# Kernel tuning notes

Measured on AMD Instinct MI355X. Metric: run time of the kernel, lower is better.

Reference implementation:

```python
import jax, jax.numpy as jnp
import numpy as np

C = 256        # in_channels == depth
HEADS = 8
K = 251        # kernel_size == attended axis length
DH = C // HEADS  # 32
EPS = 1e-5


def _bn(x, g, b, axes, ch_axis):
    # training-mode batchnorm: batch statistics, biased variance
    m = jnp.mean(x, axes, keepdims=True)
    v = jnp.var(x, axes, keepdims=True)
    shape = [1] * x.ndim
    shape[ch_axis] = -1
    return (x - m) / jnp.sqrt(v + EPS) * g.reshape(shape) + b.reshape(shape)


def _axial_cross(x, y, wk, wq, wv, gk, bk, gq, bq, gkq, bkq, glog, blog, rel):
    B, _, H, W = x.shape  # [B, C, H, W], height_dim=False -> attend over W
    # permute(0,2,1,3) then fold freq axis into batch: [B*H, C, W]
    xb = x.transpose(0, 2, 1, 3).reshape(B * H, C, W)
    yb = y.transpose(0, 2, 1, 3).reshape(B * H, C, W)
    # 1x1 conv1d == channel-mixing einsum, then BN over (batch, length)
    k = _bn(jnp.einsum('oc,bcl->bol', wk, xb), gk, bk, (0, 2), 1)
    q = _bn(jnp.einsum('oc,bcl->bol', wq, yb), gq, bq, (0, 2), 1)
    v = _bn(jnp.einsum('oc,bcl->bol', wv, xb), gkq, bkq, (0, 2), 1)  # original uses kq_bn on v
    kqv = jnp.concatenate([k, q, v], axis=1).reshape(B * H, HEADS, DH * 2, W)
    k = kqv[:, :, : DH // 2]          # [b, h, dh/2, W]
    q = kqv[:, :, DH // 2: DH]        # [b, h, dh/2, W]
    v = kqv[:, :, DH:]                # [b, h, dh,   W]
    # relative position encodings gathered by distance
    ki = jnp.arange(K)
    dist = (ki[None, :] - ki[:, None] + K - 1).reshape(-1)
    rel_e = rel[:, dist].reshape(DH * 2, K, K)
    q_enc = rel_e[: DH // 2]
    k_enc = rel_e[DH // 2: DH]
    v_enc = rel_e[DH:]
    qk = jnp.einsum('bhdx,bhdy->bhxy', q, k)
    qr = jnp.einsum('bhdx,dxy->bhxy', q, q_enc)
    kr = jnp.einsum('bhdx,dxy->bhxy', k, k_enc).transpose(0, 1, 3, 2)
    logits = jnp.concatenate([qk, qr, kr], axis=1)  # [b, 3*h, W, W]
    logits = _bn(logits, glog, blog, (0, 2, 3), 1)  # BatchNorm2d on 3*h channels
    logits = logits.reshape(B * H, 3, HEADS, W, W).sum(axis=1)
    weights = jax.nn.softmax(logits, axis=3)
    attn = jnp.einsum('bhxy,bhdy->bhdx', weights, v)        # [b, h, dh, W]
    attn_enc = jnp.einsum('bhxy,dxy->bhdx', weights, v_enc)  # [b, h, dh, W]
    attn_out = jnp.concatenate([attn, attn_enc], axis=-1)    # cat along length axis (as in original)
    attn_out = attn_out.reshape(B * H, C * 2, W)
    out = attn_out.reshape(B, H, C, 2, W).sum(axis=3)        # [B, H, C, W]
    return out.transpose(0, 2, 1, 3)                          # [B, C, H, W]


def setup_inputs() -> dict:
    key = jax.random.key(0)
    ks = jax.random.split(key, 6)
    B, H, W = 2, 15, 251
    sc = 0.05
    return {
        'x': jax.random.normal(ks[0], (B, C, H, W), jnp.float32),
        'y': jax.random.normal(ks[1], (B, C, H, W), jnp.float32),
        'wk': jax.random.normal(ks[2], (C // 2, C), jnp.float32) * sc,
        'wq': jax.random.normal(ks[3], (C // 2, C), jnp.float32) * sc,
        'wv': jax.random.normal(ks[4], (C, C), jnp.float32) * sc,
        'gk': jnp.ones((C // 2,), jnp.float32), 'bk': jnp.zeros((C // 2,), jnp.float32),
        'gq': jnp.ones((C // 2,), jnp.float32), 'bq': jnp.zeros((C // 2,), jnp.float32),
        'gkq': jnp.ones((C,), jnp.float32), 'bkq': jnp.zeros((C,), jnp.float32),
        'glog': jnp.ones((HEADS * 3,), jnp.float32), 'blog': jnp.zeros((HEADS * 3,), jnp.float32),
        'rel': jax.random.normal(ks[5], (DH * 2, 2 * K - 1), jnp.float32),
    }


def reference(x, y, wk, wq, wv, gk, bk, gq, bq, gkq, bkq, glog, blog, rel):
    return _axial_cross(x, y, wk, wq, wv, gk, bk, gq, bq, gkq, bkq, glog, blog, rel)
```

## Files before the change

### kernel.cpp

```cpp
#include <hip/hip_runtime.h>
#include <hip/hip_bf16.h>
#include <cstdint>

#define WPOS 251
#define NBB  30
#define NCH  512
#define RELP 501
#define NEPS 1e-5f

typedef _Float16 half2_t __attribute__((ext_vector_type(2)));
typedef _Float16 half8_t __attribute__((ext_vector_type(8)));
typedef float f32x16_t __attribute__((ext_vector_type(16)));

#if defined(__has_builtin)
#if __has_builtin(__builtin_amdgcn_fdot2)
#define FDOT2(a, b, c) __builtin_amdgcn_fdot2((a), (b), (c), false)
#endif
#endif
#ifndef FDOT2
#define FDOT2(a, b, c) ((float)(a)[0] * (float)(b)[0] + (float)(a)[1] * (float)(b)[1] + (c))
#endif

static constexpr size_t SZ_Z     = (size_t)NBB * NCH * WPOS;
static constexpr size_t OFF_Z    = 0;
static constexpr size_t OFF_VH   = OFF_Z + SZ_Z;
static constexpr size_t SZ_VH    = (size_t)NBB * 8 * 128 * 32;
static constexpr size_t OFF_RETC = OFF_VH + SZ_VH;
static constexpr size_t OFF_VETP = OFF_RETC + (size_t)RELP * 16;
static constexpr size_t OFF_P1Q  = OFF_VETP + (size_t)256 * 32;
static constexpr size_t OFF_P1K  = OFF_P1Q + (size_t)16 * 502;
static constexpr size_t OFF_P2Q  = OFF_P1K + (size_t)16 * 502;
static constexpr size_t OFF_P2K  = OFF_P2Q + (size_t)256 * 502;
static constexpr size_t OFF_CA   = OFF_P2K + (size_t)256 * 502;
static constexpr size_t OFF_CB   = OFF_CA + 512;
static constexpr size_t OFF_LP   = OFF_CB + 512;
static constexpr size_t OFF_LAB  = OFF_LP + (size_t)240 * 6;
static constexpr size_t OFF_LPP  = OFF_LAB + 48;

static __device__ __forceinline__ unsigned packh2(float a, float b) {
  half2_t t;
  t[0] = (_Float16)a;
  t[1] = (_Float16)b;
  return __builtin_bit_cast(unsigned, t);
}
static __device__ __forceinline__ half2_t ash2(unsigned u) {
  return __builtin_bit_cast(half2_t, u);
}

__global__ __launch_bounds__(256) void k_gemm(
    const float* __restrict__ x, const float* __restrict__ y,
    const float* __restrict__ wk, const float* __restrict__ wq,
    const float* __restrict__ wv, float* __restrict__ z) {
  int l0 = blockIdx.x * 64;
  int o0 = blockIdx.y * 64;
  int bb = blockIdx.z;
  int b = bb / 15, hi = bb % 15;
  const float* src;
  const float* wmat;
  int orow0;
  if (o0 < 128)      { wmat = wk; orow0 = o0;       src = x; }
  else if (o0 < 256) { wmat = wq; orow0 = o0 - 128; src = y; }
  else               { wmat = wv; orow0 = o0 - 256; src = x; }

  __shared__ _Float16 Ah[64][68];
  __shared__ _Float16 Bh[64][68];

  int tid = threadIdx.x;
  int lane = tid & 63, wv4 = tid >> 6;
  int wo = wv4 >> 1, wl = wv4 & 1;
  int m = lane & 31, kh = lane >> 5;

  f32x16_t acc = {};

  int cA = tid & 63, ogA = tid >> 6;
  int lB = tid & 63, kgB = tid >> 6;
  int lglob = l0 + lB;
  bool lok = (lglob < WPOS);
  const float* xcol = src + (size_t)(((size_t)b * 256) * 15 + hi) * WPOS + lglob;

  for (int c0 = 0; c0 < 256; c0 += 64) {
#pragma unroll
    for (int i = 0; i < 16; ++i) {
      int o = ogA * 16 + i;
      Ah[o][cA] = (_Float16)wmat[(size_t)(orow0 + o) * 256 + c0 + cA];
    }
#pragma unroll
    for (int i = 0; i < 16; ++i) {
      int k = kgB * 16 + i;
      float v = lok ? xcol[(size_t)(c0 + k) * 15 * WPOS] : 0.f;
      Bh[k][lB] = (_Float16)v;
    }
    __syncthreads();
#pragma unroll
    for (int ks = 0; ks < 4; ++ks) {
      const _Float16* ap = &Ah[wo * 32 + m][ks * 16 + kh * 8];
      uint2 aLo = *(const uint2*)(ap);
      uint2 aHi = *(const uint2*)(ap + 4);
      uint4 au = {aLo.x, aLo.y, aHi.x, aHi.y};
      half8_t af = __builtin_bit_cast(half8_t, au);
      half8_t bf;
      int kb = ks * 16 + kh * 8;
      int bcol = wl * 32 + m;
#pragma unroll
      for (int e = 0; e < 8; ++e) bf[e] = Bh[kb + e][bcol];
      acc = __builtin_amdgcn_mfma_f32_32x32x16_f16(af, bf, acc, 0, 0, 0);
    }
    __syncthreads();
  }

  int n = lane & 31;
  int lout = l0 + wl * 32 + n;
  if (lout < WPOS) {
#pragma unroll
    for (int r = 0; r < 16; ++r) {
      int mrow = (r & 3) + 8 * (r >> 2) + 4 * kh;
      int o = o0 + wo * 32 + mrow;
      z[((size_t)bb * NCH + o) * WPOS + lout] = acc[r];
    }
  }
}

__global__ __launch_bounds__(256) void k_chan_stats(
    const float* __restrict__ z,
    const float* __restrict__ gk, const float* __restrict__ bk,
    const float* __restrict__ gq, const float* __restrict__ bq,
    const float* __restrict__ gkq, const float* __restrict__ bkq,
    float* __restrict__ ca, float* __restrict__ cb) {
  int o = blockIdx.x;
  int tid = threadIdx.x;
  float s = 0.f, s2 = 0.f;
  for (int idx = tid; idx < NBB * WPOS; idx += 256) {
    int bb = idx / WPOS, l = idx - bb * WPOS;
    float v = z[((size_t)bb * NCH + o) * WPOS + l];
    s += v; s2 += v * v;
  }
  __shared__ float r1[256], r2[256];
  r1[tid] = s; r2[tid] = s2; __syncthreads();
  for (int st = 128; st > 0; st >>= 1) {
    if (tid < st) { r1[tid] += r1[tid + st]; r2[tid] += r2[tid + st]; }
    __syncthreads();
  }
  if (tid == 0) {
    float n = (float)(NBB * WPOS);
    float mean = r1[0] / n;
    float var = r2[0] / n - mean * mean;
    float g, bi;
    if (o < 128)      { g = gk[o];        bi = bk[o]; }
    else if (o < 256) { g = gq[o - 128];  bi = bq[o - 128]; }
    else              { g = gkq[o - 256]; bi = bkq[o - 256]; }
    float a = g / sqrtf(var + NEPS);
    ca[o] = a;
    cb[o] = bi - mean * a;
  }
}

__global__ __launch_bounds__(256) void k_norm_vh(
    const float* __restrict__ z, const float* __restrict__ ca, const float* __restrict__ cb,
    unsigned* __restrict__ vh) {
  int blk = blockIdx.x;
  int bbh = blk % 240, lt = blk / 240;
  int bb = bbh >> 3, h = bbh & 7;
  int l0 = lt * 64;
  __shared__ float T[32][65];
  int tid = threadIdx.x;
  const float* zv = z + ((size_t)bb * NCH + h * 64 + 32) * WPOS;
  for (int i = tid; i < 32 * 64; i += 256) {
    int ch = i >> 6, l = i & 63;
    int gl = l0 + l;
    int cch = h * 64 + 32 + ch;
    T[ch][l] = (gl < WPOS) ? (ca[cch] * zv[(size_t)ch * WPOS + gl] + cb[cch]) : 0.f;
  }
  __syncthreads();
  int p0 = l0 >> 1;
  for (int i = tid; i < 32 * 32; i += 256) {
    int pl = i >> 5, ch = i & 31;
    int gp = p0 + pl;
    if (gp < 128)
      vh[((size_t)bbh * 128 + gp) * 32 + ch] = packh2(T[ch][2 * pl], T[ch][2 * pl + 1]);
  }
}

__global__ void k_rel_prep(const float* __restrict__ rel, unsigned* __restrict__ retc,
                           unsigned* __restrict__ vetp) {
  int idx = blockIdx.x * 256 + threadIdx.x;
  if (idx < RELP * 16) {
    int p = idx >> 4, j = idx & 15;
    float lo, hi;
    if (j < 8) {
      lo = rel[(size_t)(2 * j) * RELP + p];
      hi = rel[(size_t)(2 * j + 1) * RELP + p];
    } else {
      int jj = j - 8;
      lo = rel[(size_t)(16 + 2 * jj) * RELP + (500 - p)];
      hi = rel[(size_t)(17 + 2 * jj) * RELP + (500 - p)];
    }
    retc[(size_t)p * 16 + j] = packh2(lo, hi);
  } else {
    int i2 = idx - RELP * 16;
    if (i2 >= 256 * 32) return;
    int t = i2 >> 5, ch = i2 & 31;
    float lo = (2 * t <= 500) ? rel[(size_t)(32 + ch) * RELP + 2 * t] : 0.f;
    float hi = (2 * t + 1 <= 500) ? rel[(size_t)(32 + ch) * RELP + 2 * t + 1] : 0.f;
    vetp[(size_t)t * 32 + ch] = packh2(lo, hi);
  }
}

__global__ __launch_bounds__(256) void k_prefix(const float* __restrict__ rel,
                                                float* __restrict__ p1q, float* __restrict__ p1k,
                                                float* __restrict__ p2q, float* __restrict__ p2k) {
  int task = blockIdx.x;
  const float* ra;
  const float* rb = nullptr;
  float* outp;
  if (task < 16)        { ra = rel + (size_t)task * RELP; outp = p1q + (size_t)task * 502; }
  else if (task < 32)   { ra = rel + (size_t)task * RELP; outp = p1k + (size_t)(task - 16) * 502; }
  else if (task < 288)  { int pr = task - 32;
                          ra = rel + (size_t)(pr >> 4) * RELP;
                          rb = rel + (size_t)(pr & 15) * RELP;
                          outp = p2q + (size_t)pr * 502; }
  else                  { int pr = task - 288;
                          ra = rel + (size_t)(16 + (pr >> 4)) * RELP;
                          rb = rel + (size_t)(16 + (pr & 15)) * RELP;
                          outp = p2k + (size_t)pr * 502; }
  __shared__ float buf[256];
  int t = threadIdx.x;
  int i0 = 2 * t, i1 = 2 * t + 1;
  float a0 = (i0 < RELP) ? (rb ? ra[i0] * rb[i0] : ra[i0]) : 0.f;
  float a1 = (i1 < RELP) ? (rb ? ra[i1] * rb[i1] : ra[i1]) : 0.f;
  buf[t] = a0 + a1;
  __syncthreads();
#pragma unroll
  for (int off = 1; off < 256; off <<= 1) {
    float v = buf[t];
    float add = (t >= off) ? buf[t - off] : 0.f;
    __syncthreads();
    buf[t] = v + add;
    __syncthreads();
  }
  float ex = buf[t] - (a0 + a1);
  if (i0 <= RELP) outp[i0] = ex;
  if (i1 <= RELP) outp[i1] = ex + a0;
}

__device__ __forceinline__ float block_reduce(float v, float* red, int tid) {
  red[tid] = v; __syncthreads();
  for (int s = 128; s > 0; s >>= 1) {
    if (tid < s) red[tid] += red[tid + s];
    __syncthreads();
  }
  float r = red[0]; __syncthreads();
  return r;
}

__global__ __launch_bounds__(256) void k_lstats1(
    const float* __restrict__ z, const float* __restrict__ ca, const float* __restrict__ cb,
    const float* __restrict__ p1q, const float* __restrict__ p1k,
    const float* __restrict__ p2q, const float* __restrict__ p2k,
    float* __restrict__ lpp) {
  int blk = blockIdx.x;
  int bbh = blk % 240, xc = blk / 240;
  int bb = bbh >> 3, h = bbh & 7;
  int x0 = xc * 64;
  int tid = threadIdx.x;
  __shared__ float qs[16][68], ks[16][68];
  __shared__ float red[256];
  const float* zb = z + ((size_t)bb * NCH + h * 64) * WPOS;
  for (int idx = tid; idx < 16 * 64; idx += 256) {
    int d = idx >> 6, xl = idx & 63;
    int xg = x0 + xl;
    float kv = 0.f, qv = 0.f;
    if (xg < WPOS) {
      int chk = h * 64 + d, chq = h * 64 + 16 + d;
      kv = ca[chk] * zb[(size_t)d * WPOS + xg] + cb[chk];
      qv = ca[chq] * zb[(size_t)(16 + d) * WPOS + xg] + cb[chq];
    }
    ks[d][xl] = kv; qs[d][xl] = qv;
  }
  __syncthreads();
  float* outp = lpp + ((size_t)bbh * 4 + xc) * 548;
  if (tid < 16) {
    float s = 0.f;
    for (int xl = 0; xl < 64; ++xl) s += qs[tid][xl];
    outp[516 + tid] = s;
  } else if (tid < 32) {
    float s = 0.f;
    for (int xl = 0; xl < 64; ++xl) s += ks[tid - 16][xl];
    outp[532 + (tid - 16)] = s;
  }
  {
    int d = tid >> 4, d2 = tid & 15;
    float g1 = 0.f, g2 = 0.f;
    for (int xl = 0; xl < 64; ++xl) {
      g1 += qs[d][xl] * qs[d2][xl];
      g2 += ks[d][xl] * ks[d2][xl];
    }
    outp[tid] = g1;
    outp[256 + tid] = g2;
  }
  float v_sumqr = 0.f, v_sqqr = 0.f, v_sumkr = 0.f, v_sqkr = 0.f;
  for (int idx = tid; idx < 16 * 64; idx += 256) {
    int d = idx >> 6, xl = idx & 63;
    int xg = x0 + xl;
    if (xg < WPOS) {
      int ihi = 501 - xg, ilo = 250 - xg;
      float qv = qs[d][xl];
      v_sumqr += qv * (p1q[d * 502 + ihi] - p1q[d * 502 + ilo]);
      float t = 0.f;
      for (int d2 = 0; d2 < 16; ++d2) {
        const float* pp = p2q + (size_t)(d * 16 + d2) * 502;
        t += qs[d2][xl] * (pp[ihi] - pp[ilo]);
      }
      v_sqqr += qv * t;
      float kv = ks[d][xl];
      v_sumkr += kv * (p1k[d * 502 + ihi] - p1k[d * 502 + ilo]);
      float t2 = 0.f;
      for (int d2 = 0; d2 < 16; ++d2) {
        const float* pp = p2k + (size_t)(d * 16 + d2) * 502;
        t2 += ks[d2][xl] * (pp[ihi] - pp[ilo]);
      }
      v_sqkr += kv * t2;
    }
  }
  float r1 = block_reduce(v_sumqr, red, tid);
  float r2 = block_reduce(v_sqqr, red, tid);
  float r3 = block_reduce(v_sumkr, red, tid);
  float r4 = block_reduce(v_sqkr, red, tid);
  if (tid == 0) { outp[512] = r1; outp[513] = r2; outp[514] = r3; outp[515] = r4; }
}

__global__ __launch_bounds__(256) void k_lstats2(const float* __restrict__ lpp,
                                                 float* __restrict__ lp) {
  int bbh = blockIdx.x;
  int tid = threadIdx.x;
  __shared__ float red[256];
  __shared__ float qsums[16], ksums[16];
  const float* b0 = lpp + (size_t)bbh * 4 * 548;
  float qg = b0[tid] + b0[548 + tid] + b0[1096 + tid] + b0[1644 + tid];
  float kg = b0[256 + tid] + b0[804 + tid] + b0[1352 + tid] + b0[1900 + tid];
  if (tid < 16) {
    qsums[tid] = b0[516 + tid] + b0[1064 + tid] + b0[1612 + tid] + b0[2160 + tid];
    ksums[tid] = b0[532 + tid] + b0[1080 + tid] + b0[1628 + tid] + b0[2176 + tid];
  }
  float sqqk = block_reduce(qg * kg, red, tid);
  if (tid == 0) {
    float sum_qk = 0.f;
    for (int d = 0; d < 16; ++d) sum_qk += qsums[d] * ksums[d];
    float s1 = 0.f, s2 = 0.f, s3 = 0.f, s4 = 0.f;
    for (int c = 0; c < 4; ++c) {
      const float* bc = b0 + (size_t)c * 548;
      s1 += bc[512]; s2 += bc[513]; s3 += bc[514]; s4 += bc[515];
    }
    float* o = lp + (size_t)bbh * 6;
    o[0] = sum_qk; o[1] = sqqk;
    o[2] = s1; o[3] = s2; o[4] = s3; o[5] = s4;
  }
}

__global__ void k_logit_final(const float* __restrict__ lp,
                              const float* __restrict__ glog, const float* __restrict__ blog,
                              float* __restrict__ lab) {
  int c = threadIdx.x;
  if (c >= 24) return;
  int grp = c >> 3, h = c & 7;
  float s = 0.f, s2 = 0.f;
  for (int bb = 0; bb < NBB; ++bb) {
    const float* o = lp + (size_t)(bb * 8 + h) * 6 + grp * 2;
    s += o[0]; s2 += o[1];
  }
  float n = (float)NBB * (float)WPOS * (float)WPOS;
  float mean = s / n;
  float var = s2 / n - mean * mean;
  float la = glog[c] / sqrtf(var + NEPS);
  lab[c * 2] = la;
  lab[c * 2 + 1] = blog[c] - mean * la;
}

__global__ __launch_bounds__(256) void k_attn(
    const float* __restrict__ z, const float* __restrict__ ca, const float* __restrict__ cb,
    const unsigned* __restrict__ vh,
    const unsigned* __restrict__ retc, const unsigned* __restrict__ vetp,
    const float* __restrict__ lab, float* __restrict__ out) {
  int blk = blockIdx.x;
  int bbh = blk % 240, tile = blk / 240;
  int bb = bbh >> 3, h = bbh & 7;
  int b = bb / 15, hi = bb % 15;
  int x0 = tile * 32;
  int nr = min(32, WPOS - x0);
  int tid = threadIdx.x;
  int lane = tid & 63, wvid = tid >> 6;

  const float LOG2E = 1.4426950408889634f;
  float la_qk = lab[h * 2] * LOG2E;
  float la_qr = lab[(8 + h) * 2] * LOG2E;
  float la_kr = lab[(16 + h) * 2] * LOG2E;

  __shared__ __align__(16) unsigned Su[32 * 132];
  __shared__ __align__(16) unsigned winU[282 * 18];
  __shared__ __align__(16) unsigned uSh[256];
  _Float16* S = (_Float16*)Su;
  unsigned* qsP = uSh;
  float* sred = (float*)uSh;
  float* Cred = (float*)winU;

  int pwin0 = 251 - x0 - nr;
  int nwin = 250 + nr;

  const float* zb = z + ((size_t)bb * NCH + h * 64) * WPOS;

  for (int i = tid; i < nwin * 16; i += 256) {
    int r = i >> 4, j = i & 15;
    winU[r * 18 + j] = retc[(size_t)(pwin0 + r) * 16 + j];
  }

  {
    int xx = tid & 31, j = tid >> 5;
    int xcl = min(x0 + xx, WPOS - 1);
    int ch0 = h * 64 + 16 + 2 * j;
    float q0 = ca[ch0]     * zb[(size_t)(16 + 2 * j) * WPOS + xcl] + cb[ch0];
    float q1 = ca[ch0 + 1] * zb[(size_t)(17 + 2 * j) * WPOS + xcl] + cb[ch0 + 1];
    qsP[xx * 8 + j] = packh2(q0, q1);
  }

  int yy = wvid * 64 + lane;
  int yc = min(yy, WPOS - 1);
  bool yok = (yy < WPOS);
  half2_t khv[8];
#pragma unroll
  for (int d = 0; d < 8; ++d) {
    int ch = h * 64 + 2 * d;
    float k0 = ca[ch]     * zb[(size_t)(2 * d) * WPOS + yc] + cb[ch];
    float k1 = ca[ch + 1] * zb[(size_t)(2 * d + 1) * WPOS + yc] + cb[ch + 1];
    khv[d] = __builtin_bit_cast(half2_t, packh2(k0, k1));
  }
  __syncthreads();

  {
    int rowbase = yc + nr - 1;
    for (int xx = 0; xx < nr; ++xx) {
      const unsigned* wr = &winU[(size_t)(rowbase - xx) * 18];
      const unsigned* qp = &qsP[xx * 8];
      float dqk = 0.f, dqr = 0.f, dkr = 0.f;
#pragma unroll
      for (int j2 = 0; j2 < 4; ++j2) {
        uint2 ue = *(const uint2*)(wr + 2 * j2);
        uint2 uk = *(const uint2*)(wr + 8 + 2 * j2);
        uint2 uq = *(const uint2*)(qp + 2 * j2);
        half2_t qe0 = ash2(ue.x), qe1 = ash2(ue.y);
        half2_t ke0 = ash2(uk.x), ke1 = ash2(uk.y);
        half2_t q0  = ash2(uq.x), q1  = ash2(uq.y);
        half2_t k0 = khv[2 * j2], k1 = khv[2 * j2 + 1];
        dqk = FDOT2(q0, k0, dqk);  dqk = FDOT2(q1, k1, dqk);
        dqr = FDOT2(q0, qe0, dqr); dqr = FDOT2(q1, qe1, dqr);
        dkr = FDOT2(k0, ke0, dkr); dkr = FDOT2(k1, ke1, dkr);
      }
      float sval = la_qk * dqk + la_qr * dqr + la_kr * dkr;
      S[xx * 264 + yy] = yok ? (_Float16)sval : (_Float16)0.f;
    }
  }
  for (int i = tid; i < 32 * 8; i += 256)
    S[(i >> 3) * 264 + 256 + (i & 7)] = (_Float16)0.f;
  if (nr < 32) {
    int ntail = (32 - nr) * 264;
    for (int i = tid; i < ntail; i += 256) S[nr * 264 + i] = (_Float16)0.f;
  }
  __syncthreads();

  int xx = lane & 31;
  int sl = wvid * 2 + (lane >> 5);
  int ylo = sl * 32;
  const unsigned* Srp = Su + xx * 132;
  {
    float m = -1e30f;
    if (sl < 7) {
#pragma unroll
      for (int pp = 0; pp < 16; ++pp) {
        half2_t hp = ash2(Srp[(ylo >> 1) + pp]);
        m = fmaxf(m, fmaxf((float)hp[0], (float)hp[1]));
      }
    } else {
#pragma unroll
      for (int pp = 0; pp < 13; ++pp) {
        half2_t hp = ash2(Srp[112 + pp]);
        m = fmaxf(m, fmaxf((float)hp[0], (float)hp[1]));
      }
      m = fmaxf(m, (float)S[xx * 264 + 250]);
    }
    sred[sl * 32 + xx] = m;
  }
  __syncthreads();
  float rowm = sred[0 * 32 + xx];
#pragma unroll
  for (int s = 1; s < 8; ++s) rowm = fmaxf(rowm, sred[s * 32 + xx]);
  __syncthreads();
  {
    float sacc = 0.f;
    unsigned* Swp = Su + xx * 132;
    if (sl < 7) {
#pragma unroll
      for (int pp = 0; pp < 16; ++pp) {
        half2_t hp = ash2(Swp[(ylo >> 1) + pp]);
        float e0 = exp2f((float)hp[0] - rowm);
        float e1 = exp2f((float)hp[1] - rowm);
        Swp[(ylo >> 1) + pp] = packh2(e0, e1);
        sacc += e0 + e1;
      }
    } else {
#pragma unroll
      for (int pp = 0; pp < 13; ++pp) {
        half2_t hp = ash2(Swp[112 + pp]);
        float e0 = exp2f((float)hp[0] - rowm);
        float e1 = exp2f((float)hp[1] - rowm);
        Swp[112 + pp] = packh2(e0, e1);
        sacc += e0 + e1;
      }
      float e = exp2f((float)S[xx * 264 + 250] - rowm);
      S[xx * 264 + 250] = (_Float16)e;
      sacc += e;
    }
    sred[sl * 32 + xx] = sacc;
  }
  __syncthreads();
  float denom = 0.f;
#pragma unroll
  for (int s = 0; s < 8; ++s) denom += sred[s * 32 + xx];

  f32x16_t acc = {};
  int xcol = lane & 31;
  int khh = lane >> 5;
  const _Float16* Srow = S + xcol * 264;
  {
    const unsigned* vhb = vh + (size_t)bbh * 128 * 32 + xcol;
#pragma unroll
    for (int ks = 0; ks < 4; ++ks) {
      int y0 = 64 * wvid + 16 * ks + 8 * khh;
      int t0 = y0 >> 1;
      uint4 au = {vhb[(size_t)(t0 + 0) * 32], vhb[(size_t)(t0 + 1) * 32],
                  vhb[(size_t)(t0 + 2) * 32], vhb[(size_t)(t0 + 3) * 32]};
      half8_t af = __builtin_bit_cast(half8_t, au);
      half8_t bf = *(const half8_t*)(Srow + y0);
      acc = __builtin_amdgcn_mfma_f32_32x32x16_f16(af, bf, acc, 0, 0, 0);
    }
    const unsigned* vpb = vetp + xcol;
    int ybase = xcol + x0 - 250;
#pragma unroll
    for (int ks = 0; ks < 8; ++ks) {
      int p0 = 128 * wvid + 16 * ks + 8 * khh;
      int t0 = p0 >> 1;
      uint4 au = {vpb[(size_t)(t0 + 0) * 32], vpb[(size_t)(t0 + 1) * 32],
                  vpb[(size_t)(t0 + 2) * 32], vpb[(size_t)(t0 + 3) * 32]};
      half8_t af = __builtin_bit_cast(half8_t, au);
      half8_t bf;
#pragma unroll
      for (int e = 0; e < 8; ++e) {
        int yv = ybase + p0 + e;
        bf[e] = ((unsigned)yv < 264u) ? Srow[yv] : (_Float16)0.f;
      }
      acc = __builtin_amdgcn_mfma_f32_32x32x16_f16(af, bf, acc, 0, 0, 0);
    }
  }

  if (wvid > 0) {
    float* cp = Cred + ((size_t)(wvid - 1) * 64 + lane) * 17;
#pragma unroll
    for (int r = 0; r < 16; ++r) cp[r] = acc[r];
  }
  __syncthreads();
  if (wvid == 0) {
#pragma unroll
    for (int w2 = 0; w2 < 3; ++w2) {
      const float* cp = Cred + ((size_t)w2 * 64 + lane) * 17;
#pragma unroll
      for (int r = 0; r < 16; ++r) acc[r] += cp[r];
    }
    if (xcol < nr) {
      float rinv = 1.0f / denom;
      int xg = x0 + xcol;
#pragma unroll
      for (int r = 0; r < 16; ++r) {
        int d = (r & 3) + 8 * (r >> 2) + 4 * khh;
        out[(((size_t)b * 256 + h * 32 + d) * 15 + hi) * WPOS + xg] = acc[r] * rinv;
      }
    }
  }
}

extern "C" void kernel_launch(void* const* d_in, const int* in_sizes, int n_in,
                              void* d_out, int out_size, void* d_ws, size_t ws_size,
                              hipStream_t stream) {
  const float* x    = (const float*)d_in[0];
  const float* y    = (const float*)d_in[1];
  const float* wk   = (const float*)d_in[2];
  const float* wq   = (const float*)d_in[3];
  const float* wv   = (const float*)d_in[4];
  const float* gk   = (const float*)d_in[5];
  const float* bk   = (const float*)d_in[6];
  const float* gq   = (const float*)d_in[7];
  const float* bq   = (const float*)d_in[8];
  const float* gkq  = (const float*)d_in[9];
  const float* bkq  = (const float*)d_in[10];
  const float* glog = (const float*)d_in[11];
  const float* blog = (const float*)d_in[12];
  const float* rel  = (const float*)d_in[13];
  float* out = (float*)d_out;
  float* ws  = (float*)d_ws;

  float* z      = ws + OFF_Z;
  unsigned* vh  = (unsigned*)(ws + OFF_VH);
  unsigned* retc= (unsigned*)(ws + OFF_RETC);
  unsigned* vetp= (unsigned*)(ws + OFF_VETP);
  float* p1q    = ws + OFF_P1Q;
  float* p1k    = ws + OFF_P1K;
  float* p2q    = ws + OFF_P2Q;
  float* p2k    = ws + OFF_P2K;
  float* ca     = ws + OFF_CA;
  float* cb     = ws + OFF_CB;
  float* lp     = ws + OFF_LP;
  float* lab    = ws + OFF_LAB;
  float* lpp    = ws + OFF_LPP;

  dim3 g1(4, 8, NBB);
  k_gemm<<<g1, 256, 0, stream>>>(x, y, wk, wq, wv, z);
  k_chan_stats<<<512, 256, 0, stream>>>(z, gk, bk, gq, bq, gkq, bkq, ca, cb);
  k_norm_vh<<<960, 256, 0, stream>>>(z, ca, cb, vh);
  k_rel_prep<<<(RELP * 16 + 256 * 32 + 255) / 256, 256, 0, stream>>>(rel, retc, vetp);
  k_prefix<<<544, 256, 0, stream>>>(rel, p1q, p1k, p2q, p2k);
  k_lstats1<<<960, 256, 0, stream>>>(z, ca, cb, p1q, p1k, p2q, p2k, lpp);
  k_lstats2<<<240, 256, 0, stream>>>(lpp, lp);
  k_logit_final<<<1, 32, 0, stream>>>(lp, glog, blog, lab);
  k_attn<<<240 * 8, 256, 0, stream>>>(z, ca, cb, vh, retc, vetp, lab, out);
}
```

Before: 113.9 us.

## Fuse BN statistics into GEMM epilogue and merge small kernels to cut launches

Per-channel sum and sum-of-squares are now computed in the GEMM epilogue via wave shuffles and atomics, which removes the separate channel-stats pass over z. The rel-prep and prefix kernels are merged into one launch, the V-normalise and logit-stats kernels are merged into k_mid, and the logit BN finalisation now happens inside k_attn using atomically accumulated totals. The kernel count drops from nine to five plus a memset. In exchange the atomics make the float sums order-nondeterministic, and each block recomputes the affine coefficients.

```diff
diff --git a/kernel.cpp b/kernel.cpp
--- a/kernel.cpp
+++ b/kernel.cpp
@@ -31,11 +31,8 @@
 static constexpr size_t OFF_P1K  = OFF_P1Q + (size_t)16 * 502;
 static constexpr size_t OFF_P2Q  = OFF_P1K + (size_t)16 * 502;
 static constexpr size_t OFF_P2K  = OFF_P2Q + (size_t)256 * 502;
-static constexpr size_t OFF_CA   = OFF_P2K + (size_t)256 * 502;
-static constexpr size_t OFF_CB   = OFF_CA + 512;
-static constexpr size_t OFF_LP   = OFF_CB + 512;
-static constexpr size_t OFF_LAB  = OFF_LP + (size_t)240 * 6;
-static constexpr size_t OFF_LPP  = OFF_LAB + 48;
+static constexpr size_t OFF_LPP  = OFF_P2K + (size_t)256 * 502;
+static constexpr size_t OFF_ACC  = OFF_LPP + (size_t)960 * 548;
 
 static __device__ __forceinline__ unsigned packh2(float a, float b) {
   half2_t t;
@@ -47,168 +44,35 @@
   return __builtin_bit_cast(half2_t, u);
 }
 
-__global__ __launch_bounds__(256) void k_gemm(
-    const float* __restrict__ x, const float* __restrict__ y,
-    const float* __restrict__ wk, const float* __restrict__ wq,
-    const float* __restrict__ wv, float* __restrict__ z) {
-  int l0 = blockIdx.x * 64;
-  int o0 = blockIdx.y * 64;
-  int bb = blockIdx.z;
-  int b = bb / 15, hi = bb % 15;
-  const float* src;
-  const float* wmat;
-  int orow0;
-  if (o0 < 128)      { wmat = wk; orow0 = o0;       src = x; }
-  else if (o0 < 256) { wmat = wq; orow0 = o0 - 128; src = y; }
-  else               { wmat = wv; orow0 = o0 - 256; src = x; }
-
-  __shared__ _Float16 Ah[64][68];
-  __shared__ _Float16 Bh[64][68];
-
-  int tid = threadIdx.x;
-  int lane = tid & 63, wv4 = tid >> 6;
-  int wo = wv4 >> 1, wl = wv4 & 1;
-  int m = lane & 31, kh = lane >> 5;
-
-  f32x16_t acc = {};
-
-  int cA = tid & 63, ogA = tid >> 6;
-  int lB = tid & 63, kgB = tid >> 6;
-  int lglob = l0 + lB;
-  bool lok = (lglob < WPOS);
-  const float* xcol = src + (size_t)(((size_t)b * 256) * 15 + hi) * WPOS + lglob;
-
-  for (int c0 = 0; c0 < 256; c0 += 64) {
-#pragma unroll
-    for (int i = 0; i < 16; ++i) {
-      int o = ogA * 16 + i;
-      Ah[o][cA] = (_Float16)wmat[(size_t)(orow0 + o) * 256 + c0 + cA];
-    }
-#pragma unroll
-    for (int i = 0; i < 16; ++i) {
-      int k = kgB * 16 + i;
-      float v = lok ? xcol[(size_t)(c0 + k) * 15 * WPOS] : 0.f;
-      Bh[k][lB] = (_Float16)v;
-    }
-    __syncthreads();
-#pragma unroll
-    for (int ks = 0; ks < 4; ++ks) {
-      const _Float16* ap = &Ah[wo * 32 + m][ks * 16 + kh * 8];
-      uint2 aLo = *(const uint2*)(ap);
-      uint2 aHi = *(const uint2*)(ap + 4);
-      uint4 au = {aLo.x, aLo.y, aHi.x, aHi.y};
-      half8_t af = __builtin_bit_cast(half8_t, au);
-      half8_t bf;
-      int kb = ks * 16 + kh * 8;
-      int bcol = wl * 32 + m;
-#pragma unroll
-      for (int e = 0; e < 8; ++e) bf[e] = Bh[kb + e][bcol];
-      acc = __builtin_amdgcn_mfma_f32_32x32x16_f16(af, bf, acc, 0, 0, 0);
-    }
-    __syncthreads();
-  }
-
-  int n = lane & 31;
-  int lout = l0 + wl * 32 + n;
-  if (lout < WPOS) {
-#pragma unroll
-    for (int r = 0; r < 16; ++r) {
-      int mrow = (r & 3) + 8 * (r >> 2) + 4 * kh;
-      int o = o0 + wo * 32 + mrow;
-      z[((size_t)bb * NCH + o) * WPOS + lout] = acc[r];
-    }
-  }
-}
-
-__global__ __launch_bounds__(256) void k_chan_stats(
-    const float* __restrict__ z,
-    const float* __restrict__ gk, const float* __restrict__ bk,
-    const float* __restrict__ gq, const float* __restrict__ bq,
-    const float* __restrict__ gkq, const float* __restrict__ bkq,
-    float* __restrict__ ca, float* __restrict__ cb) {
-  int o = blockIdx.x;
-  int tid = threadIdx.x;
-  float s = 0.f, s2 = 0.f;
-  for (int idx = tid; idx < NBB * WPOS; idx += 256) {
-    int bb = idx / WPOS, l = idx - bb * WPOS;
-    float v = z[((size_t)bb * NCH + o) * WPOS + l];
-    s += v; s2 += v * v;
-  }
-  __shared__ float r1[256], r2[256];
-  r1[tid] = s; r2[tid] = s2; __syncthreads();
-  for (int st = 128; st > 0; st >>= 1) {
-    if (tid < st) { r1[tid] += r1[tid + st]; r2[tid] += r2[tid + st]; }
-    __syncthreads();
-  }
-  if (tid == 0) {
-    float n = (float)(NBB * WPOS);
-    float mean = r1[0] / n;
-    float var = r2[0] / n - mean * mean;
-    float g, bi;
-    if (o < 128)      { g = gk[o];        bi = bk[o]; }
-    else if (o < 256) { g = gq[o - 128];  bi = bq[o - 128]; }
-    else              { g = gkq[o - 256]; bi = bkq[o - 256]; }
-    float a = g / sqrtf(var + NEPS);
-    ca[o] = a;
-    cb[o] = bi - mean * a;
-  }
-}
-
-__global__ __launch_bounds__(256) void k_norm_vh(
-    const float* __restrict__ z, const float* __restrict__ ca, const float* __restrict__ cb,
-    unsigned* __restrict__ vh) {
+__global__ __launch_bounds__(256) void k_pre(
+    const float* __restrict__ rel, unsigned* __restrict__ retc, unsigned* __restrict__ vetp,
+    float* __restrict__ p1q, float* __restrict__ p1k,
+    float* __restrict__ p2q, float* __restrict__ p2k) {
   int blk = blockIdx.x;
-  int bbh = blk % 240, lt = blk / 240;
-  int bb = bbh >> 3, h = bbh & 7;
-  int l0 = lt * 64;
-  __shared__ float T[32][65];
-  int tid = threadIdx.x;
-  const float* zv = z + ((size_t)bb * NCH + h * 64 + 32) * WPOS;
-  for (int i = tid; i < 32 * 64; i += 256) {
-    int ch = i >> 6, l = i & 63;
-    int gl = l0 + l;
-    int cch = h * 64 + 32 + ch;
-    T[ch][l] = (gl < WPOS) ? (ca[cch] * zv[(size_t)ch * WPOS + gl] + cb[cch]) : 0.f;
-  }
-  __syncthreads();
-  int p0 = l0 >> 1;
-  for (int i = tid; i < 32 * 32; i += 256) {
-    int pl = i >> 5, ch = i & 31;
-    int gp = p0 + pl;
-    if (gp < 128)
-      vh[((size_t)bbh * 128 + gp) * 32 + ch] = packh2(T[ch][2 * pl], T[ch][2 * pl + 1]);
-  }
-}
-
-__global__ void k_rel_prep(const float* __restrict__ rel, unsigned* __restrict__ retc,
-                           unsigned* __restrict__ vetp) {
-  int idx = blockIdx.x * 256 + threadIdx.x;
-  if (idx < RELP * 16) {
-    int p = idx >> 4, j = idx & 15;
-    float lo, hi;
-    if (j < 8) {
-      lo = rel[(size_t)(2 * j) * RELP + p];
-      hi = rel[(size_t)(2 * j + 1) * RELP + p];
-    } else {
-      int jj = j - 8;
-      lo = rel[(size_t)(16 + 2 * jj) * RELP + (500 - p)];
-      hi = rel[(size_t)(17 + 2 * jj) * RELP + (500 - p)];
-    }
-    retc[(size_t)p * 16 + j] = packh2(lo, hi);
-  } else {
-    int i2 = idx - RELP * 16;
-    if (i2 >= 256 * 32) return;
-    int t = i2 >> 5, ch = i2 & 31;
-    float lo = (2 * t <= 500) ? rel[(size_t)(32 + ch) * RELP + 2 * t] : 0.f;
-    float hi = (2 * t + 1 <= 500) ? rel[(size_t)(32 + ch) * RELP + 2 * t + 1] : 0.f;
-    vetp[(size_t)t * 32 + ch] = packh2(lo, hi);
-  }
-}
-
-__global__ __launch_bounds__(256) void k_prefix(const float* __restrict__ rel,
-                                                float* __restrict__ p1q, float* __restrict__ p1k,
-                                                float* __restrict__ p2q, float* __restrict__ p2k) {
-  int task = blockIdx.x;
+  if (blk < 64) {
+    int idx = blk * 256 + threadIdx.x;
+    if (idx < RELP * 16) {
+      int p = idx >> 4, j = idx & 15;
+      float lo, hi;
+      if (j < 8) {
+        lo = rel[(size_t)(2 * j) * RELP + p];
+        hi = rel[(size_t)(2 * j + 1) * RELP + p];
+      } else {
+        int jj = j - 8;
+        lo = rel[(size_t)(16 + 2 * jj) * RELP + (500 - p)];
+        hi = rel[(size_t)(17 + 2 * jj) * RELP + (500 - p)];
+      }
+      retc[(size_t)p * 16 + j] = packh2(lo, hi);
+    } else if (idx < RELP * 16 + 256 * 32) {
+      int i2 = idx - RELP * 16;
+      int t = i2 >> 5, ch = i2 & 31;
+      float lo = (2 * t <= 500) ? rel[(size_t)(32 + ch) * RELP + 2 * t] : 0.f;
+      float hi = (2 * t + 1 <= 500) ? rel[(size_t)(32 + ch) * RELP + 2 * t + 1] : 0.f;
+      vetp[(size_t)t * 32 + ch] = packh2(lo, hi);
+    }
+    return;
+  }
+  int task = blk - 64;
   const float* ra;
   const float* rb = nullptr;
   float* outp;
@@ -242,6 +106,97 @@
   if (i1 <= RELP) outp[i1] = ex + a0;
 }
 
+__global__ __launch_bounds__(256) void k_gemm(
+    const float* __restrict__ x, const float* __restrict__ y,
+    const float* __restrict__ wk, const float* __restrict__ wq,
+    const float* __restrict__ wv, float* __restrict__ z,
+    float* __restrict__ csum, float* __restrict__ csum2) {
+  int l0 = blockIdx.x * 64;
+  int o0 = blockIdx.y * 64;
+  int bb = blockIdx.z;
+  int b = bb / 15, hi = bb % 15;
+  const float* src;
+  const float* wmat;
+  int orow0;
+  if (o0 < 128)      { wmat = wk; orow0 = o0;       src = x; }
+  else if (o0 < 256) { wmat = wq; orow0 = o0 - 128; src = y; }
+  else               { wmat = wv; orow0 = o0 - 256; src = x; }
+
+  __shared__ _Float16 Ah[64][68];
+  __shared__ _Float16 Bh[64][68];
+
+  int tid = threadIdx.x;
+  int lane = tid & 63, wv4 = tid >> 6;
+  int wo = wv4 >> 1, wl = wv4 & 1;
+  int m = lane & 31, kh = lane >> 5;
+
+  f32x16_t acc = {};
+
+  int cA = tid & 63, ogA = tid >> 6;
+  int lB = tid & 63, kgB = tid >> 6;
+  int lglob = l0 + lB;
+  bool lok = (lglob < WPOS);
+  const float* xcol = src + (size_t)(((size_t)b * 256) * 15 + hi) * WPOS + lglob;
+
+  for (int c0 = 0; c0 < 256; c0 += 64) {
+#pragma unroll
+    for (int i = 0; i < 16; ++i) {
+      int o = ogA * 16 + i;
+      Ah[o][cA] = (_Float16)wmat[(size_t)(orow0 + o) * 256 + c0 + cA];
+    }
+#pragma unroll
+    for (int i = 0; i < 16; ++i) {
+      int k = kgB * 16 + i;
+      float v = lok ? xcol[(size_t)(c0 + k) * 15 * WPOS] : 0.f;
+      Bh[k][lB] = (_Float16)v;
+    }
+    __syncthreads();
+#pragma unroll
+    for (int ks = 0; ks < 4; ++ks) {
+      const _Float16* ap = &Ah[wo * 32 + m][ks * 16 + kh * 8];
+      uint2 aLo = *(const uint2*)(ap);
+      uint2 aHi = *(const uint2*)(ap + 4);
+      uint4 au = {aLo.x, aLo.y, aHi.x, aHi.y};
+      half8_t af = __builtin_bit_cast(half8_t, au);
+      half8_t bf;
+      int kb = ks * 16 + kh * 8;
+      int bcol = wl * 32 + m;
+#pragma unroll
+      for (int e = 0; e < 8; ++e) bf[e] = Bh[kb + e][bcol];
+      acc = __builtin_amdgcn_mfma_f32_32x32x16_f16(af, bf, acc, 0, 0, 0);
+    }
+    __syncthreads();
+  }
+
+  int n = lane & 31;
+  int lout = l0 + wl * 32 + n;
+  if (lout < WPOS) {
+#pragma unroll
+    for (int r = 0; r < 16; ++r) {
+      int mrow = (r & 3) + 8 * (r >> 2) + 4 * kh;
+      int o = o0 + wo * 32 + mrow;
+      z[((size_t)bb * NCH + o) * WPOS + lout] = acc[r];
+    }
+  }
+
+#pragma unroll
+  for (int r = 0; r < 16; ++r) {
+    float s = acc[r];
+    float s2 = s * s;
+#pragma unroll
+    for (int m2 = 1; m2 < 32; m2 <<= 1) {
+      s  += __shfl_xor(s, m2, 64);
+      s2 += __shfl_xor(s2, m2, 64);
+    }
+    if (n == 0) {
+      int mrow = (r & 3) + 8 * (r >> 2) + 4 * kh;
+      int o = o0 + wo * 32 + mrow;
+      atomicAdd(&csum[o], s);
+      atomicAdd(&csum2[o], s2);
+    }
+  }
+}
+
 __device__ __forceinline__ float block_reduce(float v, float* red, int tid) {
   red[tid] = v; __syncthreads();
   for (int s = 128; s > 0; s >>= 1) {
@@ -252,32 +207,84 @@
   return r;
 }
 
-__global__ __launch_bounds__(256) void k_lstats1(
-    const float* __restrict__ z, const float* __restrict__ ca, const float* __restrict__ cb,
+__device__ __forceinline__ void chan_affine(
+    int ch, const float* gk, const float* bk, const float* gq, const float* bq,
+    const float* gkq, const float* bkq, const float* csum, const float* csum2,
+    float& a, float& bout) {
+  float g, bi;
+  if (ch < 128)      { g = gk[ch];        bi = bk[ch]; }
+  else if (ch < 256) { g = gq[ch - 128];  bi = bq[ch - 128]; }
+  else               { g = gkq[ch - 256]; bi = bkq[ch - 256]; }
+  float n = (float)(NBB * WPOS);
+  float mean = csum[ch] / n;
+  float var = csum2[ch] / n - mean * mean;
+  a = g / sqrtf(var + NEPS);
+  bout = bi - mean * a;
+}
+
+__global__ __launch_bounds__(256) void k_mid(
+    const float* __restrict__ z,
+    const float* __restrict__ gk, const float* __restrict__ bk,
+    const float* __restrict__ gq, const float* __restrict__ bq,
+    const float* __restrict__ gkq, const float* __restrict__ bkq,
+    const float* __restrict__ csum, const float* __restrict__ csum2,
+    unsigned* __restrict__ vh,
     const float* __restrict__ p1q, const float* __restrict__ p1k,
     const float* __restrict__ p2q, const float* __restrict__ p2k,
     float* __restrict__ lpp) {
   int blk = blockIdx.x;
-  int bbh = blk % 240, xc = blk / 240;
+  bool isV = (blk < 960);
+  int sblk = isV ? blk : blk - 960;
+  int bbh = sblk % 240, sub = sblk / 240;
   int bb = bbh >> 3, h = bbh & 7;
-  int x0 = xc * 64;
   int tid = threadIdx.x;
-  __shared__ float qs[16][68], ks[16][68];
+
+  __shared__ __align__(16) float pool[16 * 68 * 2];
   __shared__ float red[256];
+  __shared__ float caL[32], cbL[32];
+
+  if (tid < 32) {
+    int ch = h * 64 + (isV ? 32 + tid : tid);
+    chan_affine(ch, gk, bk, gq, bq, gkq, bkq, csum, csum2, caL[tid], cbL[tid]);
+  }
+  __syncthreads();
+
+  if (isV) {
+    float (*T)[65] = (float(*)[65])pool;
+    int l0 = sub * 64;
+    const float* zv = z + ((size_t)bb * NCH + h * 64 + 32) * WPOS;
+    for (int i = tid; i < 32 * 64; i += 256) {
+      int ch = i >> 6, l = i & 63;
+      int gl = l0 + l;
+      T[ch][l] = (gl < WPOS) ? (caL[ch] * zv[(size_t)ch * WPOS + gl] + cbL[ch]) : 0.f;
+    }
+    __syncthreads();
+    int p0 = l0 >> 1;
+    for (int i = tid; i < 32 * 32; i += 256) {
+      int pl = i >> 5, ch = i & 31;
+      int gp = p0 + pl;
+      if (gp < 128)
+        vh[((size_t)bbh * 128 + gp) * 32 + ch] = packh2(T[ch][2 * pl], T[ch][2 * pl + 1]);
+    }
+    return;
+  }
+
+  float (*qs)[68] = (float(*)[68])pool;
+  float (*ks)[68] = (float(*)[68])(pool + 16 * 68);
+  int x0 = sub * 64;
   const float* zb = z + ((size_t)bb * NCH + h * 64) * WPOS;
   for (int idx = tid; idx < 16 * 64; idx += 256) {
     int d = idx >> 6, xl = idx & 63;
     int xg = x0 + xl;
     float kv = 0.f, qv = 0.f;
     if (xg < WPOS) {
-      int chk = h * 64 + d, chq = h * 64 + 16 + d;
-      kv = ca[chk] * zb[(size_t)d * WPOS + xg] + cb[chk];
-      qv = ca[chq] * zb[(size_t)(16 + d) * WPOS + xg] + cb[chq];
+      kv = caL[d] * zb[(size_t)d * WPOS + xg] + cbL[d];
+      qv = caL[16 + d] * zb[(size_t)(16 + d) * WPOS + xg] + cbL[16 + d];
     }
     ks[d][xl] = kv; qs[d][xl] = qv;
   }
   __syncthreads();
-  float* outp = lpp + ((size_t)bbh * 4 + xc) * 548;
+  float* outp = lpp + ((size_t)bbh * 4 + sub) * 548;
   if (tid < 16) {
     float s = 0.f;
     for (int xl = 0; xl < 64; ++xl) s += qs[tid][xl];
@@ -329,8 +336,9 @@
 }
 
 __global__ __launch_bounds__(256) void k_lstats2(const float* __restrict__ lpp,
-                                                 float* __restrict__ lp) {
+                                                 float* __restrict__ lacc) {
   int bbh = blockIdx.x;
+  int h = bbh & 7;
   int tid = threadIdx.x;
   __shared__ float red[256];
   __shared__ float qsums[16], ksums[16];
@@ -350,36 +358,25 @@
       const float* bc = b0 + (size_t)c * 548;
       s1 += bc[512]; s2 += bc[513]; s3 += bc[514]; s4 += bc[515];
     }
-    float* o = lp + (size_t)bbh * 6;
-    o[0] = sum_qk; o[1] = sqqk;
-    o[2] = s1; o[3] = s2; o[4] = s3; o[5] = s4;
-  }
-}
-
-__global__ void k_logit_final(const float* __restrict__ lp,
-                              const float* __restrict__ glog, const float* __restrict__ blog,
-                              float* __restrict__ lab) {
-  int c = threadIdx.x;
-  if (c >= 24) return;
-  int grp = c >> 3, h = c & 7;
-  float s = 0.f, s2 = 0.f;
-  for (int bb = 0; bb < NBB; ++bb) {
-    const float* o = lp + (size_t)(bb * 8 + h) * 6 + grp * 2;
-    s += o[0]; s2 += o[1];
-  }
-  float n = (float)NBB * (float)WPOS * (float)WPOS;
-  float mean = s / n;
-  float var = s2 / n - mean * mean;
-  float la = glog[c] / sqrtf(var + NEPS);
-  lab[c * 2] = la;
-  lab[c * 2 + 1] = blog[c] - mean * la;
+    atomicAdd(&lacc[(0 * 8 + h) * 2 + 0], sum_qk);
+    atomicAdd(&lacc[(0 * 8 + h) * 2 + 1], sqqk);
+    atomicAdd(&lacc[(1 * 8 + h) * 2 + 0], s1);
+    atomicAdd(&lacc[(1 * 8 + h) * 2 + 1], s2);
+    atomicAdd(&lacc[(2 * 8 + h) * 2 + 0], s3);
+    atomicAdd(&lacc[(2 * 8 + h) * 2 + 1], s4);
+  }
 }
 
 __global__ __launch_bounds__(256) void k_attn(
-    const float* __restrict__ z, const float* __restrict__ ca, const float* __restrict__ cb,
+    const float* __restrict__ z,
+    const float* __restrict__ gk, const float* __restrict__ bk,
+    const float* __restrict__ gq, const float* __restrict__ bq,
+    const float* __restrict__ gkq, const float* __restrict__ bkq,
+    const float* __restrict__ csum, const float* __restrict__ csum2,
     const unsigned* __restrict__ vh,
     const unsigned* __restrict__ retc, const unsigned* __restrict__ vetp,
-    const float* __restrict__ lab, float* __restrict__ out) {
+    const float* __restrict__ lacc, const float* __restrict__ glog,
+    float* __restrict__ out) {
   int blk = blockIdx.x;
   int bbh = blk % 240, tile = blk / 240;
   int bb = bbh >> 3, h = bbh & 7;
@@ -390,13 +387,11 @@
   int lane = tid & 63, wvid = tid >> 6;
 
   const float LOG2E = 1.4426950408889634f;
-  float la_qk = lab[h * 2] * LOG2E;
-  float la_qr = lab[(8 + h) * 2] * LOG2E;
-  float la_kr = lab[(16 + h) * 2] * LOG2E;
 
   __shared__ __align__(16) unsigned Su[32 * 132];
   __shared__ __align__(16) unsigned winU[282 * 18];
   __shared__ __align__(16) unsigned uSh[256];
+  __shared__ float affL[68];
   _Float16* S = (_Float16*)Su;
   unsigned* qsP = uSh;
   float* sred = (float*)uSh;
@@ -405,6 +400,20 @@
   int pwin0 = 251 - x0 - nr;
   int nwin = 250 + nr;
 
+  if (tid < 32) {
+    int ch = h * 64 + tid;
+    chan_affine(ch, gk, bk, gq, bq, gkq, bkq, csum, csum2, affL[tid], affL[32 + tid]);
+  } else if (tid < 35) {
+    int grp = tid - 32;
+    int c = grp * 8 + h;
+    float n = (float)NBB * (float)WPOS * (float)WPOS;
+    float mean = lacc[c * 2] / n;
+    float var = lacc[c * 2 + 1] / n - mean * mean;
+    affL[64 + grp] = glog[c] / sqrtf(var + NEPS) * LOG2E;
+  }
+  __syncthreads();
+  float la_qk = affL[64], la_qr = affL[65], la_kr = affL[66];
+
   const float* zb = z + ((size_t)bb * NCH + h * 64) * WPOS;
 
   for (int i = tid; i < nwin * 16; i += 256) {
@@ -415,9 +424,8 @@
   {
     int xx = tid & 31, j = tid >> 5;
     int xcl = min(x0 + xx, WPOS - 1);
-    int ch0 = h * 64 + 16 + 2 * j;
-    float q0 = ca[ch0]     * zb[(size_t)(16 + 2 * j) * WPOS + xcl] + cb[ch0];
-    float q1 = ca[ch0 + 1] * zb[(size_t)(17 + 2 * j) * WPOS + xcl] + cb[ch0 + 1];
+    float q0 = affL[16 + 2 * j] * zb[(size_t)(16 + 2 * j) * WPOS + xcl] + affL[48 + 2 * j];
+    float q1 = affL[17 + 2 * j] * zb[(size_t)(17 + 2 * j) * WPOS + xcl] + affL[49 + 2 * j];
     qsP[xx * 8 + j] = packh2(q0, q1);
   }
 
@@ -427,9 +435,8 @@
   half2_t khv[8];
 #pragma unroll
   for (int d = 0; d < 8; ++d) {
-    int ch = h * 64 + 2 * d;
-    float k0 = ca[ch]     * zb[(size_t)(2 * d) * WPOS + yc] + cb[ch];
-    float k1 = ca[ch + 1] * zb[(size_t)(2 * d + 1) * WPOS + yc] + cb[ch + 1];
+    float k0 = affL[2 * d]     * zb[(size_t)(2 * d) * WPOS + yc] + affL[32 + 2 * d];
+    float k1 = affL[2 * d + 1] * zb[(size_t)(2 * d + 1) * WPOS + yc] + affL[33 + 2 * d];
     khv[d] = __builtin_bit_cast(half2_t, packh2(k0, k1));
   }
   __syncthreads();
@@ -599,7 +606,6 @@
   const float* gkq  = (const float*)d_in[9];
   const float* bkq  = (const float*)d_in[10];
   const float* glog = (const float*)d_in[11];
-  const float* blog = (const float*)d_in[12];
   const float* rel  = (const float*)d_in[13];
   float* out = (float*)d_out;
   float* ws  = (float*)d_ws;
@@ -612,20 +618,18 @@
   float* p1k    = ws + OFF_P1K;
   float* p2q    = ws + OFF_P2Q;
   float* p2k    = ws + OFF_P2K;
-  float* ca     = ws + OFF_CA;
-  float* cb     = ws + OFF_CB;
-  float* lp     = ws + OFF_LP;
-  float* lab    = ws + OFF_LAB;
   float* lpp    = ws + OFF_LPP;
-
+  float* csum   = ws + OFF_ACC;
+  float* csum2  = csum + 512;
+  float* lacc   = csum2 + 512;
+
+  hipMemsetAsync(csum, 0, (512 + 512 + 48) * sizeof(float), stream);
+  k_pre<<<608, 256, 0, stream>>>(rel, retc, vetp, p1q, p1k, p2q, p2k);
   dim3 g1(4, 8, NBB);
-  k_gemm<<<g1, 256, 0, stream>>>(x, y, wk, wq, wv, z);
-  k_chan_stats<<<512, 256, 0, stream>>>(z, gk, bk, gq, bq, gkq, bkq, ca, cb);
-  k_norm_vh<<<960, 256, 0, stream>>>(z, ca, cb, vh);
-  k_rel_prep<<<(RELP * 16 + 256 * 32 + 255) / 256, 256, 0, stream>>>(rel, retc, vetp);
-  k_prefix<<<544, 256, 0, stream>>>(rel, p1q, p1k, p2q, p2k);
-  k_lstats1<<<960, 256, 0, stream>>>(z, ca, cb, p1q, p1k, p2q, p2k, lpp);
-  k_lstats2<<<240, 256, 0, stream>>>(lpp, lp);
-  k_logit_final<<<1, 32, 0, stream>>>(lp, glog, blog, lab);
-  k_attn<<<240 * 8, 256, 0, stream>>>(z, ca, cb, vh, retc, vetp, lab, out);
-}
+  k_gemm<<<g1, 256, 0, stream>>>(x, y, wk, wq, wv, z, csum, csum2);
+  k_mid<<<1920, 256, 0, stream>>>(z, gk, bk, gq, bq, gkq, bkq, csum, csum2,
+                                  vh, p1q, p1k, p2q, p2k, lpp);
+  k_lstats2<<<240, 256, 0, stream>>>(lpp, lacc);
+  k_attn<<<240 * 8, 256, 0, stream>>>(z, gk, bk, gq, bq, gkq, bkq, csum, csum2,
+                                      vh, retc, vetp, lacc, glog, out);
+}
```

After: 159.9 us. 1.4x slower.
